# Performance work log

Measured on AMD Instinct MI355X. Metric: run time of the kernel, lower is better.

The kernel has to match this reference:

```python
import jax, jax.numpy as jnp
import numpy as np

LEAK = 0.2

def leaky(x):
    return jnp.where(x > 0, x, LEAK * x)

def relu(x):
    return jnp.maximum(x, 0)

def conv1d(x, w):
    # x [B,Cin,L], w [Cout,Cin,3], stride 1, padding 1
    return jax.lax.conv_general_dilated(x, w, (1,), [(1, 1)],
        dimension_numbers=('NCH', 'OIH', 'NCH'))

def conv2d(x, w, pad, dil=1, groups=1):
    return jax.lax.conv_general_dilated(x, w, (1, 1), [(pad, pad), (pad, pad)],
        rhs_dilation=(dil, dil), feature_group_count=groups,
        dimension_numbers=('NCHW', 'OIHW', 'NCHW'))

def bn2d(x, p, eps=1e-5):
    # p: [4,C] = gamma, beta, running_mean, running_var (eval-mode BN)
    g, b, m, v = p
    s = (1, -1, 1, 1)
    return (x - m.reshape(s)) * (g.reshape(s) / jnp.sqrt(v.reshape(s) + eps)) + b.reshape(s)

def layernorm(x, g, b, eps=1e-5):
    mu = x.mean(-1, keepdims=True)
    var = ((x - mu) ** 2).mean(-1, keepdims=True)
    return (x - mu) / jnp.sqrt(var + eps) * g + b

def l2n(x, axis, eps):
    n = jnp.sqrt((x * x).sum(axis, keepdims=True))
    return x / jnp.maximum(n, eps)


def setup_inputs() -> dict:
    key = jax.random.key(0)
    B, C, H, W = 4, 64, 48, 48
    D, Fn, T, V = 256, 8, 4, 16
    E = 16  # orthogonal prototype embed dim
    ks = iter(jax.random.split(key, 64))
    def rn(shape, s=0.05):
        return jax.random.normal(next(ks), shape, jnp.float32) * s
    def bnp(c):
        return jnp.stack([1.0 + rn((c,), 0.1), rn((c,), 0.1), rn((c,), 0.1), 1.0 + jnp.abs(rn((c,), 0.1))])
    return dict(
        basis_vector_bank=jax.random.normal(next(ks), (T, V, D), jnp.float32),
        task_f=jax.random.normal(next(ks), (B, C, 16, 16), jnp.float32),
        img_f=jax.random.normal(next(ks), (B, C, H, W), jnp.float32),
        protos=jax.random.normal(next(ks), (T, E), jnp.float32),
        tA_w1=rn((E // 4, 1, 3)), tA_w2=rn((E // 2, E // 4, 3)),
        iA_w=rn((E // 2, C, 3, 3)), iA_bn=bnp(E // 2),
        at_w1=rn((E, Fn // 2 * E)), at_b1=rn((Fn // 2 * E,)),
        at_ln_g=jnp.ones((Fn // 2 * E,)), at_ln_b=jnp.zeros((Fn // 2 * E,)),
        at_w2=rn((Fn // 2 * E, Fn * E)), at_b2=rn((Fn * E,)),
        bv_t1=rn((D // 4, 1, 3)), bv_t2=rn((D // 2, D // 4, 3)),
        bv_ic1=rn((D // 4, C, 3, 3)), bv_bn1=bnp(D // 4),
        bv_ic2=rn((D // 2, D // 4, 3, 3)), bv_bn2=bnp(D // 2),
        bv_w1=rn((D, D // 4)), bv_b1=rn((D // 4,)),
        bv_ln_g=jnp.ones((D // 4,)), bv_ln_b=jnp.zeros((D // 4,)),
        bv_w2=rn((D // 4, D)), bv_b2=rn((D,)),
        m1_w1=rn((D, D // 4)), m1_b1=rn((D // 4,)),
        m1_ln_g=jnp.ones((D // 4,)), m1_ln_b=jnp.zeros((D // 4,)),
        m1_w2=rn((D // 4, C * C)), m1_b2=rn((C * C,)),
        m3_w1=rn((D, D // 4)), m3_b1=rn((D // 4,)),
        m3_ln_g=jnp.ones((D // 4,)), m3_ln_b=jnp.zeros((D // 4,)),
        m3_w2=rn((D // 4, 9 * C * C)), m3_b2=rn((9 * C * C,)),
        blr_bn=bnp(C),
        zc_w=rn((C, C, 1, 1), 0.01), zc_b=rn((C,), 0.01),
    )


def _forward(basis_vector_bank, task_f, img_f, protos, tA_w1, tA_w2, iA_w, iA_bn,
             at_w1, at_b1, at_ln_g, at_ln_b, at_w2, at_b2,
             bv_t1, bv_t2, bv_ic1, bv_bn1, bv_ic2, bv_bn2,
             bv_w1, bv_b1, bv_ln_g, bv_ln_b, bv_w2, bv_b2,
             m1_w1, m1_b1, m1_ln_g, m1_ln_b, m1_w2, m1_b2,
             m3_w1, m3_b1, m3_ln_g, m3_ln_b, m3_w2, m3_b2,
             blr_bn, zc_w, zc_b):
    T, V, D = basis_vector_bank.shape
    B, C, H, W = img_f.shape
    E = protos.shape[1]
    Fn = at_w2.shape[1] // E
    tau = 0.5

    # --- A2SI routing features ---
    xt = task_f.reshape(B, 1, -1)
    t1 = conv1d(leaky(conv1d(xt, tA_w1)), tA_w2).mean(-1)          # [B,E/2]
    i1 = leaky(bn2d(conv2d(img_f, iA_w, 1), iA_bn)).mean((2, 3))   # [B,E/2]
    f1 = jnp.concatenate([t1, i1], axis=1)                         # [B,E]
    h = relu(layernorm(f1 @ at_w1 + at_b1, at_ln_g, at_ln_b))
    tif = (h @ at_w2 + at_b2).reshape(B, E, Fn)                    # [B,E,F]
    logits = jnp.einsum('te,bef->bft', l2n(protos, -1, 1e-8), l2n(tif, 1, 1e-8))  # [B,F,T]

    # hard gumbel-softmax (straight-through), fixed noise key for determinism
    u = jax.random.uniform(jax.random.key(42), logits.shape, jnp.float32, 1e-10, 1.0)
    g = -jnp.log(-jnp.log(u))
    y = jax.nn.softmax((logits + g) / tau, axis=-1)
    idx = jnp.argmax(y, axis=-1)                                   # [B,F]
    y_hard = jax.nn.one_hot(idx, T, dtype=y.dtype)
    set_type = y_hard + y - jax.lax.stop_gradient(y)

    bank_flat = basis_vector_bank.reshape(T, V * D)
    sbvb = jnp.einsum('bft,tk->bfk', set_type, bank_flat).reshape(B, Fn, V, D)

    # --- BasisV_filter: filter feature ---
    xt2 = task_f.reshape(B, C, -1)
    rms = jnp.sqrt((xt2 ** 2).mean((1, 2), keepdims=True))
    xt2 = (xt2 / (rms + 1e-8)).reshape(B, 1, -1)
    te = conv1d(leaky(conv1d(xt2, bv_t1)), bv_t2).mean(-1)         # [B,D/2]
    ie = leaky(bn2d(conv2d(img_f, bv_ic1, 1), bv_bn1))
    ie = leaky(bn2d(conv2d(ie, bv_ic2, 1), bv_bn2)).mean((2, 3))   # [B,D/2]
    ff = jnp.concatenate([te, ie], axis=1)                         # [B,D]
    ff = relu(layernorm(ff @ bv_w1 + bv_b1, bv_ln_g, bv_ln_b)) @ bv_w2 + bv_b2

    # --- per-(batch,type) group gather/top-k/scatter, vectorized ---
    # group bank = bank of first filter with that type (hard one-hot -> type's bank)
    occ = idx[:, None, :] == jnp.arange(T)[None, :, None]          # [B,T,F]
    first = jnp.argmax(occ, axis=-1)                               # [B,T]
    Bg = jnp.take_along_axis(sbvb, first[:, :, None, None], axis=1)  # [B,T,V,D]
    # all rows of Q within a group are identical (filter_f expanded over F),
    # so S.max(0) == cosine(ff[b], Bg[b,t])
    scores = jnp.einsum('bd,btvd->btv', l2n(ff, -1, 1e-12), l2n(Bg, -1, 1e-12))
    order = jnp.argsort(-scores, axis=-1)                          # [B,T,V] topk order
    lt = jnp.tril(jnp.ones((Fn, Fn), bool), -1)                    # j < i
    rank = ((idx[:, :, None] == idx[:, None, :]) & lt).sum(-1)     # position in group
    bidx = jnp.arange(B)[:, None]
    sel = order[bidx, idx, rank]                                   # [B,F]
    bvf = Bg[bidx, idx, sel]                                       # [B,F,D]

    # --- per-filter dynamic convolutions ---
    w1 = relu(layernorm(bvf @ m1_w1 + m1_b1, m1_ln_g, m1_ln_b)) @ m1_w2 + m1_b2
    w1 = w1.reshape(B, Fn, C, C)                                   # [B,F,out,in]
    w3 = relu(layernorm(bvf @ m3_w1 + m3_b1, m3_ln_g, m3_ln_b)) @ m3_w2 + m3_b2
    w3 = w3.reshape(B * Fn, C, C, 3, 3)

    dp0 = jnp.einsum('bfoc,bchw->bfohw', w1, img_f)                # 1x1 branch
    xin = jnp.broadcast_to(img_f[:, None], (B, Fn, C, H, W)).reshape(1, B * Fn * C, H, W)
    ker = w3.reshape(B * Fn * C, C, 3, 3)
    dpd = [conv2d(xin, ker, d, dil=d, groups=B * Fn).reshape(B, Fn, C, H, W)
           for d in (1, 2, 3)]                                     # same-padded dilated 3x3
    t_ = idx[:, :, None, None, None]
    dp = jnp.where(t_ == 0, dp0, jnp.where(t_ == 1, dpd[0],
         jnp.where(t_ == 2, dpd[1], dpd[2])))                      # [B,F,C,H,W]

    x = leaky(bn2d(dp.reshape(B * Fn, C, H, W), blr_bn)).reshape(B, Fn, C, H, W).mean(1)
    a = conv2d(x, zc_w, 0) + zc_b.reshape(1, -1, 1, 1)
    return a + img_f


@jax.jit
def reference(basis_vector_bank, task_f, img_f, protos, tA_w1, tA_w2, iA_w, iA_bn,
              at_w1, at_b1, at_ln_g, at_ln_b, at_w2, at_b2,
              bv_t1, bv_t2, bv_ic1, bv_bn1, bv_ic2, bv_bn2,
              bv_w1, bv_b1, bv_ln_g, bv_ln_b, bv_w2, bv_b2,
              m1_w1, m1_b1, m1_ln_g, m1_ln_b, m1_w2, m1_b2,
              m3_w1, m3_b1, m3_ln_g, m3_ln_b, m3_w2, m3_b2,
              blr_bn, zc_w, zc_b):
    return _forward(basis_vector_bank, task_f, img_f, protos, tA_w1, tA_w2, iA_w, iA_bn,
                    at_w1, at_b1, at_ln_g, at_ln_b, at_w2, at_b2,
                    bv_t1, bv_t2, bv_ic1, bv_bn1, bv_ic2, bv_bn2,
                    bv_w1, bv_b1, bv_ln_g, bv_ln_b, bv_w2, bv_b2,
                    m1_w1, m1_b1, m1_ln_g, m1_ln_b, m1_w2, m1_b2,
                    m3_w1, m3_b1, m3_ln_g, m3_ln_b, m3_w2, m3_b2,
                    blr_bn, zc_w, zc_b)
```

## Files before the change

kernel.cpp:

```cpp
#include <hip/hip_runtime.h>
#include <math.h>

#define LEAKC 0.2f

#define NB 4
#define NC 64
#define LLEN 16384
#define HW 2304
#define PP 54
#define PHW 2916
#define SLABP 72
#define CP 72
#define IE1C 50

typedef __attribute__((ext_vector_type(8))) short short8;
typedef __attribute__((ext_vector_type(4))) float floatx4;

__device__ __forceinline__ float leaky(float x){ return x > 0.f ? x : LEAKC*x; }

__device__ __forceinline__ float wave_sum64(float v){
  for(int off=32;off;off>>=1) v += __shfl_xor(v,off);
  return v;
}

__device__ __forceinline__ unsigned short f2bf(float x){
  unsigned u=__float_as_uint(x);
  unsigned r=u+0x7FFFu+((u>>16)&1u);
  return (unsigned short)(r>>16);
}

__device__ __forceinline__ void threefry2x32(unsigned k0, unsigned k1, unsigned& x0, unsigned& x1){
  unsigned ks0=k0, ks1=k1, ks2=k0^k1^0x1BD11BDAu;
  x0+=ks0; x1+=ks1;
  const int rot0[4]={13,15,26,6};
  const int rot1[4]={17,29,16,24};
#define TF_APPLY(rr) {for(int r=0;r<4;r++){x0+=x1; x1=(x1<<rr[r])|(x1>>(32-rr[r])); x1^=x0;}}
  TF_APPLY(rot0); x0+=ks1; x1+=ks2+1u;
  TF_APPLY(rot1); x0+=ks2; x1+=ks0+2u;
  TF_APPLY(rot0); x0+=ks0; x1+=ks1+3u;
  TF_APPLY(rot1); x0+=ks1; x1+=ks2+4u;
  TF_APPLY(rot0); x0+=ks2; x1+=ks0+5u;
#undef TF_APPLY
}

__device__ __forceinline__ float jax_uniform128(int i){
  unsigned x0=0u, x1=(unsigned)i;
  threefry2x32(0u,42u,x0,x1);
  unsigned bits = x0 ^ x1;
  unsigned fb=(bits>>9)|0x3f800000u;
  float f=__uint_as_float(fb)-1.0f;
  float u=f*(1.0f-1e-10f)+1e-10f;
  return fmaxf(1e-10f,u);
}

__global__ __launch_bounds__(256) void k_pre(const float* __restrict__ task_f,
                      const float* __restrict__ w1A, const float* __restrict__ w1B,
                      float* __restrict__ totApart, float* __restrict__ a0A, float* __restrict__ aLA,
                      float* __restrict__ totBpart, float* __restrict__ a0B, float* __restrict__ aLB,
                      float* __restrict__ rmspart,
                      const float* __restrict__ img,
                      const float* __restrict__ w1, const float* __restrict__ w2,
                      const float* __restrict__ wa,
                      unsigned short* __restrict__ imgTP,
                      unsigned short* __restrict__ W1T, unsigned short* __restrict__ W2T,
                      unsigned short* __restrict__ WAT,
                      const float* __restrict__ mw1, const float* __restrict__ mw3,
                      const float* __restrict__ bvw1p, const float* __restrict__ bvw2p,
                      const float* __restrict__ bvt2p, const float* __restrict__ atw2p,
                      const float* __restrict__ bankp,
                      const float* __restrict__ m1w2p, const float* __restrict__ m3w2p,
                      const float* __restrict__ zcwp,
                      float* __restrict__ warm){
  if(blockIdx.x<256){
    int b=blockIdx.x>>6, seg=blockIdx.x&63;
    const float* x=task_f+b*LLEN;
    float tA[4]={0,0,0,0};
    float tB[64];
#pragma unroll
    for(int c=0;c<64;c++) tB[c]=0.f;
    float sq=0.f;
    int l=seg*256+threadIdx.x;
    {
      float xm=(l>0)?x[l-1]:0.f;
      float xc=x[l];
      float xp=(l<LLEN-1)?x[l+1]:0.f;
      sq=xc*xc;
#pragma unroll
      for(int c=0;c<4;c++){
        float a=leaky(w1A[c*3+0]*xm + w1A[c*3+1]*xc + w1A[c*3+2]*xp);
        tA[c]=a;
        if(l==0) a0A[b*4+c]=a;
        if(l==LLEN-1) aLA[b*4+c]=a;
      }
#pragma unroll
      for(int c=0;c<64;c++){
        float a=leaky(w1B[c*3+0]*xm + w1B[c*3+1]*xc + w1B[c*3+2]*xp);
        tB[c]=a;
        if(l==0) a0B[b*64+c]=a;
        if(l==LLEN-1) aLB[b*64+c]=a;
      }
    }
    sq=wave_sum64(sq);
#pragma unroll
    for(int c=0;c<4;c++) tA[c]=wave_sum64(tA[c]);
#pragma unroll
    for(int c=0;c<64;c++){
      float v=tB[c];
      for(int off=32;off;off>>=1) v+=__shfl_down(v,off);
      tB[c]=v;
    }
    __shared__ float redB[4][64];
    __shared__ float redA[4][4];
    __shared__ float redQ[4];
    int wave=threadIdx.x>>6, lane=threadIdx.x&63;
    if(lane==0){
#pragma unroll
      for(int c=0;c<64;c++) redB[wave][c]=tB[c];
#pragma unroll
      for(int c=0;c<4;c++) redA[wave][c]=tA[c];
      redQ[wave]=sq;
    }
    __syncthreads();
    if(threadIdx.x<64){
      float s=redB[0][threadIdx.x]+redB[1][threadIdx.x]+redB[2][threadIdx.x]+redB[3][threadIdx.x];
      totBpart[(size_t)(b*64+seg)*64+threadIdx.x]=s;
    } else if(threadIdx.x<68){
      int c=threadIdx.x-64;
      totApart[(b*64+seg)*4+c]=redA[0][c]+redA[1][c]+redA[2][c]+redA[3][c];
    } else if(threadIdx.x==68){
      rmspart[b*64+seg]=redQ[0]+redQ[1]+redQ[2]+redQ[3];
    }
  } else if(blockIdx.x<400){
    int blk=blockIdx.x-256;
    int b=blk/36, t=blk%36;
    int p0=t*64;
    __shared__ float tile[64][65];
    int pp=threadIdx.x&63, c4=threadIdx.x>>6;
    for(int r=0;r<16;r++){
      int c=c4*16+r;
      tile[c][pp]=img[(b*64+c)*HW + p0+pp];
    }
    __syncthreads();
    int pxl=threadIdx.x>>2, cg=(threadIdx.x&3)*16;
    unsigned out[8];
#pragma unroll
    for(int q=0;q<8;q++){
      unsigned lo=f2bf(tile[cg+2*q][pxl]);
      unsigned hi=f2bf(tile[cg+2*q+1][pxl]);
      out[q]=lo|(hi<<16);
    }
    int px=p0+pxl;
    int h=px/48, w=px-h*48;
    int poff=(h+3)*PP+(w+3);
    unsigned* dst=(unsigned*)(imgTP + ((size_t)(b*PHW+poff))*64 + cg);
#pragma unroll
    for(int q=0;q<8;q++) dst[q]=out[q];
  } else if(blockIdx.x<868){
    int n=(blockIdx.x-400)*256+threadIdx.x;
    if(n<9*64*64){
      int tap=n>>12, oc=(n>>6)&63, c=n&63;
      W1T[n]=f2bf(w1[oc*576+c*9+tap]);
    } else if(n<9*64*64+9*128*64){
      int m=n-9*64*64;
      int tap=m/8192, r=m-tap*8192, oc=r>>6, c=r&63;
      W2T[m]=f2bf(w2[oc*576+c*9+tap]);
    } else {
      int q=n-9*64*64-9*128*64;
      if(q<9*16*64){
        int tap=q>>10, r=q&1023, o=r>>6, c=r&63;
        WAT[q]=(o<8)?f2bf(wa[o*576+c*9+tap]):(unsigned short)0;
      }
    }
  } else if(blockIdx.x<932){
    int t=(blockIdx.x-868)*256+threadIdx.x;
    float a=0.f;
    for(int i=t;i*16<16384;i+=16384) a+=mw1[i*16];
    for(int i=t;i*16<16384;i+=16384) a+=mw3[i*16];
    for(int i=t;i*16<16384;i+=16384) a+=bvw1p[i*16];
    for(int i=t;i*16<16384;i+=16384) a+=bvw2p[i*16];
    for(int i=t;i*16<24576;i+=16384) a+=bvt2p[i*16];
    for(int i=t;i*16<8192;i+=16384) a+=atw2p[i*16];
    for(int i=t;i*16<16384;i+=16384) a+=bankp[i*16];
    for(int i=t;i*16<262144;i+=16384) a+=m1w2p[i*16];
    for(int i=t;i*16<2359296;i+=16384) a+=m3w2p[i*16];
    for(int i=t;i*16<4096;i+=16384) a+=zcwp[i*16];
    warm[t&1023]=a;
  } else {
    int id=(blockIdx.x-932)*256+threadIdx.x;
    uint4 z=make_uint4(0,0,0,0);
    for(int cch=id;cch<19584;cch+=4096){
      int ck=cch&7, pxid=cch>>3;
      int b=pxid/612, p=pxid-b*612;
      int h,w;
      if(p<324){ int r=p/54; w=p-r*54; h=(r<3)?r:(r+48); }
      else { int q=p-324; int r2=q/6; int cc=q-r2*6; h=3+r2; w=(cc<3)?cc:(cc+48); }
      *(uint4*)(imgTP + ((size_t)(b*PHW + h*PP + w))*64 + ck*8)=z;
    }
  }
}

__global__ __launch_bounds__(512) void k_conv12(const unsigned short* __restrict__ imgTP,
                        const unsigned short* __restrict__ W1T,
                        const unsigned short* __restrict__ W2T,
                        const unsigned short* __restrict__ WAT,
                        const float* __restrict__ bn1, const float* __restrict__ bn2,
                        const float* __restrict__ bnA,
                        float* __restrict__ iepart, float* __restrict__ i1part){
  int tid=threadIdx.x;
  int lane=tid&63, wv=tid>>6;
  int n0=lane&15, kg=lane>>4;
  if(blockIdx.x<96){
    int blk=blockIdx.x;
    int b=blk/24, hp=blk-b*24;
    int h0=hp*2;
    __shared__ unsigned short slab[6*54*SLABP];
    __shared__ unsigned short ie1[4*IE1C*CP];
    {
      const unsigned short* ibase=imgTP+((size_t)b*PHW+(size_t)(h0+1)*PP)*64;
      for(int e=tid;e<6*54*8;e+=512){
        int rr=e/(54*8), rem=e-rr*54*8, w=rem>>3, ck=rem&7;
        uint4 v=*(const uint4*)(ibase+((size_t)(rr*PP+w))*64+ck*8);
        *(uint4*)(slab+(rr*54+w)*SLABP+ck*8)=v;
      }
      if(tid<64){
        int br=tid>>4, cq=(tid>>3)&1, ck=tid&7;
        *(uint4*)(ie1+((size_t)(br*IE1C+(cq?49:0)))*CP+ck*8)=make_uint4(0,0,0,0);
      }
    }
    __syncthreads();
    {
      int mt=wv&3, rh=wv>>2;
      floatx4 acc[2][3];
#pragma unroll
      for(int rr=0;rr<2;rr++)
#pragma unroll
        for(int nt=0;nt<3;nt++) acc[rr][nt]=(floatx4){0.f,0.f,0.f,0.f};
#pragma unroll
      for(int ti=0;ti<3;ti++){
#pragma unroll
        for(int tj=0;tj<3;tj++){
          int tap=ti*3+tj;
          const unsigned short* Ab=W1T+(size_t)tap*4096;
#pragma unroll
          for(int c0=0;c0<64;c0+=32){
            short8 a=*(const short8*)(Ab+((mt*16+n0)*64+c0+kg*8));
#pragma unroll
            for(int rr=0;rr<2;rr++){
              int sr=rh*2+rr+ti;
#pragma unroll
              for(int nt=0;nt<3;nt++){
                int sc=nt*16+n0+tj+2;
                short8 bv=*(const short8*)(slab+(sr*54+sc)*SLABP+c0+kg*8);
                acc[rr][nt]=__builtin_amdgcn_mfma_f32_16x16x32_bf16(a,bv,acc[rr][nt],0,0,0);
              }
            }
          }
        }
      }
      int obase=mt*16+kg*4;
      float scale[4],m_[4],be_[4];
#pragma unroll
      for(int reg=0;reg<4;reg++){
        int o=obase+reg;
        scale[reg]=bn1[o]/sqrtf(bn1[192+o]+1e-5f);
        m_[reg]=bn1[128+o]; be_[reg]=bn1[64+o];
      }
#pragma unroll
      for(int rr=0;rr<2;rr++){
        int br=rh*2+rr;
        bool rv=((unsigned)(h0-1+br))<48u;
#pragma unroll
        for(int nt=0;nt<3;nt++){
          float v0=rv?leaky((acc[rr][nt][0]-m_[0])*scale[0]+be_[0]):0.f;
          float v1=rv?leaky((acc[rr][nt][1]-m_[1])*scale[1]+be_[1]):0.f;
          float v2=rv?leaky((acc[rr][nt][2]-m_[2])*scale[2]+be_[2]):0.f;
          float v3=rv?leaky((acc[rr][nt][3]-m_[3])*scale[3]+be_[3]):0.f;
          unsigned w0=f2bf(v0)|((unsigned)f2bf(v1)<<16);
          unsigned w1=f2bf(v2)|((unsigned)f2bf(v3)<<16);
          uint2 pk={w0,w1};
          *(uint2*)(ie1+((size_t)(br*IE1C+(nt*16+1+n0)))*CP+obase)=pk;
        }
      }
    }
    __syncthreads();
    {
      int mt2=wv;
      floatx4 acc[6];
#pragma unroll
      for(int i=0;i<6;i++) acc[i]=(floatx4){0.f,0.f,0.f,0.f};
#pragma unroll
      for(int ti=0;ti<3;ti++){
#pragma unroll
        for(int tj=0;tj<3;tj++){
          int tap=ti*3+tj;
          const unsigned short* Ab=W2T+(size_t)tap*8192;
#pragma unroll
          for(int c0=0;c0<64;c0+=32){
            short8 a=*(const short8*)(Ab+((mt2*16+n0)*64+c0+kg*8));
#pragma unroll
            for(int rr=0;rr<2;rr++){
              int sr=rr+ti;
#pragma unroll
              for(int wc=0;wc<3;wc++){
                int q=wc*16+n0+tj;
                short8 bv=*(const short8*)(ie1+((size_t)(sr*IE1C+q))*CP+c0+kg*8);
                acc[rr*3+wc]=__builtin_amdgcn_mfma_f32_16x16x32_bf16(a,bv,acc[rr*3+wc],0,0,0);
              }
            }
          }
        }
      }
      int obase=mt2*16+kg*4;
#pragma unroll
      for(int reg=0;reg<4;reg++){
        int o=obase+reg;
        float scale=bn2[o]/sqrtf(bn2[384+o]+1e-5f);
        float m_=bn2[256+o], be_=bn2[128+o];
        float part=0;
#pragma unroll
        for(int i=0;i<6;i++) part+=leaky((acc[i][reg]-m_)*scale+be_);
        for(int off=1;off<16;off<<=1) part+=__shfl_xor(part,off);
        if(n0==0) iepart[(b*24+hp)*128+o]=part*(1.f/2304.f);
      }
    }
  } else {
    int blk2=blockIdx.x-96;
    int b=blk2/3, hg=blk2-b*3;
    int hp=hg*8+wv;
    int h0=hp*2;
    const unsigned short* ib=imgTP+(size_t)b*PHW*64;
    floatx4 acc[6];
#pragma unroll
    for(int i=0;i<6;i++) acc[i]=(floatx4){0.f,0.f,0.f,0.f};
#pragma unroll
    for(int ti=0;ti<3;ti++){
#pragma unroll
      for(int tj=0;tj<3;tj++){
        int tap=ti*3+tj;
        const unsigned short* Ab=WAT+(size_t)tap*1024;
#pragma unroll
        for(int c0=0;c0<64;c0+=32){
          short8 a=*(const short8*)(Ab+(n0*64+c0+kg*8));
#pragma unroll
          for(int rr=0;rr<2;rr++){
            int r=h0+rr+ti-1+3;
#pragma unroll
            for(int wc=0;wc<3;wc++){
              int w=wc*16+n0+tj-1+3;
              short8 bv=*(const short8*)(ib+((size_t)(r*PP+w)*64+c0+kg*8));
              acc[rr*3+wc]=__builtin_amdgcn_mfma_f32_16x16x32_bf16(a,bv,acc[rr*3+wc],0,0,0);
            }
          }
        }
      }
    }
    int obase=kg*4;
#pragma unroll
    for(int reg=0;reg<4;reg++){
      int o=obase+reg;
      float part=0;
      if(o<8){
        float scale=bnA[o]/sqrtf(bnA[24+o]+1e-5f);
        float m_=bnA[16+o], be_=bnA[8+o];
#pragma unroll
        for(int i=0;i<6;i++) part+=leaky((acc[i][reg]-m_)*scale+be_);
      }
      for(int off=1;off<16;off<<=1) part+=__shfl_xor(part,off);
      if(n0==0 && o<8) i1part[(b*24+hp)*8+o]=part*(1.f/2304.f);
    }
  }
}

__global__ __launch_bounds__(512,1) void k_mid(
    const float* __restrict__ totApart, const float* __restrict__ a0A, const float* __restrict__ aLA,
    const float* __restrict__ totBpart, const float* __restrict__ a0B, const float* __restrict__ aLB,
    const float* __restrict__ rmspart,
    const float* __restrict__ tA_w2, const float* __restrict__ bv_t2,
    const float* __restrict__ i1part, const float* __restrict__ iepart,
    const float* __restrict__ at_w1, const float* __restrict__ at_b1,
    const float* __restrict__ at_ln_g, const float* __restrict__ at_ln_b,
    const float* __restrict__ at_w2, const float* __restrict__ at_b2,
    const float* __restrict__ protos,
    const float* __restrict__ bv_w1, const float* __restrict__ bv_b1,
    const float* __restrict__ bv_ln_g, const float* __restrict__ bv_ln_b,
    const float* __restrict__ bv_w2, const float* __restrict__ bv_b2,
    const float* __restrict__ bank,
    const float* __restrict__ m1_w1, const float* __restrict__ m1_b1,
    const float* __restrict__ m1_g,  const float* __restrict__ m1_bb,
    const float* __restrict__ m3_w1, const float* __restrict__ m3_b1,
    const float* __restrict__ m3_g,  const float* __restrict__ m3_bb,
    int* __restrict__ idxo, float* __restrict__ hid1, float* __restrict__ hid3){
  int b=blockIdx.x;
  int tid=threadIdx.x;
  int lane=tid&63, wv=tid>>6;
  const float invL=1.0f/16384.0f;
  __shared__ float sT[64], s0[64], sL[64];
  __shared__ float red8[64][9];
  __shared__ float iered[128], i1red[8];
  __shared__ float totA_s[4];
  __shared__ float rms_s;
  __shared__ float part[512];
  __shared__ float te_s[128], t1_s[8];
  __shared__ float f1[16], h[64], tif[128], tifn[128], tden[8], pden[4], pn[64], z[32];
  __shared__ int sidx[8], sfirst[4], srank[8], rows[8];
  __shared__ float fbuf[256], hh[64], ffn_s[256], finv_s;
  __shared__ float scores[64];
  __shared__ int order[64];
  __shared__ float bvf[2048];

  {
    int c8=tid>>3, g8=tid&7;
    float s8=0;
#pragma unroll
    for(int seg=g8*8;seg<g8*8+8;seg++) s8+=totBpart[(size_t)(b*64+seg)*64+c8];
    red8[c8][g8]=s8;
  }
  if(tid>=64 && tid<128){
    int t=tid-64;
    s0[t]=a0B[b*64+t]; sL[t]=aLB[b*64+t];
  } else if(tid>=128 && tid<192){
    float v=rmspart[b*64+(tid-128)];
    v=wave_sum64(v);
    if(tid==128) rms_s=v;
  } else if(tid>=192 && tid<196){
    int c=tid-192;
    float s=0;
#pragma unroll 8
    for(int seg=0;seg<64;seg++) s+=totApart[(b*64+seg)*4+c];
    totA_s[c]=s;
  } else if(tid>=256 && tid<384){
    int c=tid-256;
    float s=0;
#pragma unroll 8
    for(int g=0;g<24;g++) s+=iepart[(b*24+g)*128+c];
    iered[c]=s;
  } else if(tid>=384 && tid<392){
    int f=tid-384;
    float s=0;
#pragma unroll
    for(int g=0;g<24;g++) s+=i1part[(b*24+g)*8+f];
    i1red[f]=s;
  }
  __syncthreads();
  if(tid<64){
    float s=0;
#pragma unroll
    for(int g=0;g<8;g++) s+=red8[tid][g];
    sT[tid]=s;
  }
  __syncthreads();
  float scB=1.0f/(sqrtf(rms_s*invL)+1e-8f);
  if(tid<256){
    int c2=tid&127, h2=tid>>7;
    const float* wr=bv_t2+c2*192;
    float s=0;
    for(int c1=h2*32;c1<h2*32+32;c1+=8){
      float4 q[6];
      const float4* r4=(const float4*)(wr+c1*3);
#pragma unroll
      for(int u=0;u<6;u++) q[u]=r4[u];
      const float* qq=(const float*)q;
#pragma unroll
      for(int u=0;u<8;u++){
        int c=c1+u;
        float T=sT[c], A0=s0[c], AL=sL[c];
        s += qq[u*3+0]*(T-AL) + qq[u*3+1]*T + qq[u*3+2]*(T-A0);
      }
    }
    part[tid]=s;
  } else if(tid>=384 && tid<392){
    int c2=tid-384;
    float s=0;
    for(int c1=0;c1<4;c1++){
      float T=totA_s[c1], A0=a0A[b*4+c1], AL=aLA[b*4+c1];
      const float* w=&tA_w2[(c2*4+c1)*3];
      s += w[0]*(T-AL) + w[1]*T + w[2]*(T-A0);
    }
    t1_s[c2]=s*invL;
  }
  __syncthreads();
  if(tid<128) te_s[tid]=(part[tid]+part[tid+128])*invL*scB;
  __syncthreads();

  if(tid<8) f1[tid]=t1_s[tid];
  else if(tid<16) f1[tid]=i1red[tid-8];
  __syncthreads();
  if(tid<64){
    float s=at_b1[lane];
#pragma unroll
    for(int i=0;i<16;i++) s+=f1[i]*at_w1[i*64+lane];
    float mu=wave_sum64(s)*(1.f/64.f);
    float d=s-mu;
    float var=wave_sum64(d*d)*(1.f/64.f);
    h[lane]=fmaxf(d*(1.0f/sqrtf(var+1e-5f))*at_ln_g[lane]+at_ln_b[lane],0.f);
  }
  __syncthreads();
  if(tid<256){
    int n=tid&127, h2=tid>>7;
    float a0=0,a1=0;
    for(int k=h2*32;k<h2*32+32;k+=2){
      a0+=h[k]*at_w2[k*128+n];
      a1+=h[k+1]*at_w2[(k+1)*128+n];
    }
    part[tid]=a0+a1;
  }
  __syncthreads();
  if(tid<128) tif[tid]=at_b2[tid]+part[tid]+part[tid+128];
  __syncthreads();
  if(tid<8){
    int f=tid;
    float ss=0; for(int e=0;e<16;e++){float v=tif[e*8+f]; ss+=v*v;}
    tden[f]=fmaxf(sqrtf(ss),1e-8f);
  } else if(tid<12){
    int t=tid-8;
    float ss=0; for(int e=0;e<16;e++){float v=protos[t*16+e]; ss+=v*v;}
    pden[t]=fmaxf(sqrtf(ss),1e-8f);
  }
  __syncthreads();
  if(tid<128) tifn[tid]=tif[tid]/tden[tid&7];
  if(tid<64) pn[tid]=protos[tid]/pden[tid>>4];
  __syncthreads();
  if(tid<32){
    int f=tid>>2, t=tid&3;
    float ss=0;
#pragma unroll
    for(int e=0;e<16;e++) ss+=pn[t*16+e]*tifn[e*8+f];
    float u=jax_uniform128(b*32+f*4+t);
    float g=-logf(-logf(u));
    z[tid]=ss+g;
  }
  __syncthreads();
  if(tid<8){
    float best=z[tid*4]; int bi=0;
    for(int t=1;t<4;t++){ float v=z[tid*4+t]; if(v>best){best=v;bi=t;} }
    sidx[tid]=bi;
  }
  __syncthreads();
  if(tid<4){
    int t=tid;
    int fi=0;
    for(int f=7;f>=0;f--) if(sidx[f]==t) fi=f;
    sfirst[t]=fi;
  } else if(tid<12){
    int f=tid-4;
    int c=0; for(int f2=0;f2<f;f2++) if(sidx[f2]==sidx[f]) c++;
    srank[f]=c;
  }
  __syncthreads();

  if(tid<128) fbuf[tid]=te_s[tid];
  else if(tid<256) fbuf[tid]=iered[tid-128];
  __syncthreads();
  if(tid<256){
    int l64=tid&63, q=tid>>6;
    float a0=0,a1=0,a2=0,a3=0;
    for(int k=q*64;k<q*64+64;k+=4){
      a0+=fbuf[k]  *bv_w1[k*64+l64];
      a1+=fbuf[k+1]*bv_w1[(k+1)*64+l64];
      a2+=fbuf[k+2]*bv_w1[(k+2)*64+l64];
      a3+=fbuf[k+3]*bv_w1[(k+3)*64+l64];
    }
    part[tid]=((a0+a1)+(a2+a3));
  }
  __syncthreads();
  if(tid<64){
    float s=bv_b1[lane]+part[lane]+part[64+lane]+part[128+lane]+part[192+lane];
    float mu=wave_sum64(s)*(1.f/64.f);
    float d=s-mu;
    float var=wave_sum64(d*d)*(1.f/64.f);
    hh[lane]=fmaxf(d*(1.0f/sqrtf(var+1e-5f))*bv_ln_g[lane]+bv_ln_b[lane],0.f);
  }
  __syncthreads();
  {
    int n=tid&255, h2=tid>>8;
    float a0=0,a1=0;
    for(int k=h2*32;k<h2*32+32;k+=2){
      a0+=hh[k]*bv_w2[k*256+n];
      a1+=hh[k+1]*bv_w2[(k+1)*256+n];
    }
    part[tid]=a0+a1;
  }
  __syncthreads();
  if(tid<256) ffn_s[tid]=bv_b2[tid]+part[tid]+part[tid+256];
  __syncthreads();
  if(tid<64){
    float sq=0;
#pragma unroll
    for(int u=0;u<4;u++){ float v=ffn_s[u*64+lane]; sq+=v*v; }
    sq=wave_sum64(sq);
    if(lane==0) finv_s=1.0f/fmaxf(sqrtf(sq),1e-12f);
  }
  __syncthreads();
  if(tid<256) ffn_s[tid]*=finv_s;
  __syncthreads();

  if(tid<128){
    int it=tid&63, h2=tid>>6;
    int t=it>>4, v=it&15;
    int tt=sidx[sfirst[t]];
    const float4* row=(const float4*)(bank+(tt*16+v)*256);
    float sa=0,na=0;
    for(int d4=h2*32;d4<h2*32+32;d4++){
      float4 r=row[d4];
      const float* fp=&ffn_s[d4*4];
      sa+=fp[0]*r.x+fp[1]*r.y+fp[2]*r.z+fp[3]*r.w;
      na+=r.x*r.x+r.y*r.y+r.z*r.z+r.w*r.w;
    }
    part[tid]=sa;
    part[256+tid]=na;
  }
  __syncthreads();
  if(tid<64) scores[tid]=(part[tid]+part[tid+64])/fmaxf(sqrtf(part[256+tid]+part[320+tid]),1e-12f);
  __syncthreads();
  if(tid<4){
    const float* sc=&scores[tid*16];
    unsigned used=0;
    for(int pk=0;pk<16;pk++){
      int best=-1; float bv=-1e30f;
      for(int v2=0;v2<16;v2++){
        if(used&(1u<<v2)) continue;
        float vv=sc[v2];
        if(best<0||vv>bv){bv=vv;best=v2;}
      }
      used|=1u<<best;
      order[tid*16+pk]=best;
    }
  }
  __syncthreads();
  if(tid<8){
    int t=sidx[tid];
    int v=order[t*16+srank[tid]];
    rows[tid]=t*16+v;
    idxo[b*8+tid]=t;
  }
  __syncthreads();

  for(int ii=tid;ii<2048;ii+=512){
    int r=ii>>8, d=ii&255;
    bvf[ii]=bank[rows[r]*256+d];
  }
  __syncthreads();
  {
    int r=wv;
    const float* bp=&bvf[r*256];
    float a0=0,a1=0,a2=0,a3=0;
    float c0=0,c1=0,c2=0,c3=0;
    for(int d=0;d<256;d+=4){
      float b0=bp[d],b1=bp[d+1],b2=bp[d+2],b3=bp[d+3];
      a0+=b0*m1_w1[d*64+lane];
      a1+=b1*m1_w1[(d+1)*64+lane];
      a2+=b2*m1_w1[(d+2)*64+lane];
      a3+=b3*m1_w1[(d+3)*64+lane];
      c0+=b0*m3_w1[d*64+lane];
      c1+=b1*m3_w1[(d+1)*64+lane];
      c2+=b2*m3_w1[(d+2)*64+lane];
      c3+=b3*m3_w1[(d+3)*64+lane];
    }
    float s1=m1_b1[lane]+((a0+a1)+(a2+a3));
    float s3=m3_b1[lane]+((c0+c1)+(c2+c3));
    float mu=wave_sum64(s1)*(1.f/64.f);
    float dd=s1-mu;
    float var=wave_sum64(dd*dd)*(1.f/64.f);
    hid1[(b*8+r)*64+lane]=fmaxf(dd*(1.0f/sqrtf(var+1e-5f))*m1_g[lane]+m1_bb[lane],0.f);
    mu=wave_sum64(s3)*(1.f/64.f);
    dd=s3-mu;
    var=wave_sum64(dd*dd)*(1.f/64.f);
    hid3[(b*8+r)*64+lane]=fmaxf(dd*(1.0f/sqrtf(var+1e-5f))*m3_g[lane]+m3_bb[lane],0.f);
  }
}

__global__ __launch_bounds__(256) void k_heads(const float* __restrict__ hid1, const float* __restrict__ hid3,
                        const float* __restrict__ w2a, const float* __restrict__ b2a,
                        const float* __restrict__ w2b, const float* __restrict__ b2b,
                        unsigned short* __restrict__ A1, unsigned short* __restrict__ A3){
  __shared__ float hl[2048];
  if(blockIdx.x<16){
    int n=blockIdx.x*256+threadIdx.x;
    float wcol[64];
#pragma unroll
    for(int k=0;k<64;k++) wcol[k]=w2a[k*4096+n];
    float bb=b2a[n];
    for(int i=threadIdx.x;i<2048;i+=256) hl[i]=hid1[i];
    __syncthreads();
    for(int bf=0;bf<32;bf++){
      float s=bb;
#pragma unroll
      for(int k=0;k<64;k++) s+=hl[bf*64+k]*wcol[k];
      A1[bf*4096+n]=f2bf(s);
    }
  } else {
    int n=(blockIdx.x-16)*256+threadIdx.x;
    float wcol[64];
#pragma unroll
    for(int k=0;k<64;k++) wcol[k]=w2b[(size_t)k*36864+n];
    float bb=b2b[n];
    for(int i=threadIdx.x;i<2048;i+=256) hl[i]=hid3[i];
    __syncthreads();
    int o=n/576, rem=n-o*576;
    int c=rem/9, tap=rem-c*9;
    size_t base=((size_t)tap*64+o)*64+c;
    for(int bf=0;bf<32;bf++){
      float s=bb;
#pragma unroll
      for(int k=0;k<64;k++) s+=hl[bf*64+k]*wcol[k];
      A3[(size_t)bf*9*4096+base]=f2bf(s);
    }
  }
}

__global__ __launch_bounds__(512) void k_dynF(const unsigned short* __restrict__ imgTP,
                       const unsigned short* __restrict__ A1, const unsigned short* __restrict__ A3,
                       const int* __restrict__ idx, const float* __restrict__ bn,
                       const float* __restrict__ zc_w, const float* __restrict__ zc_b,
                       const float* __restrict__ img, float* __restrict__ out){
  int blk=blockIdx.x;
  int b=blk/48, r0=blk-b*48;
  int tid=threadIdx.x;
  int lane=tid&63, w8=tid>>6;
  int mt=w8&3, fh=w8>>2;
  int n0=lane&15, kg=lane>>4;
  __shared__ unsigned short slab[7*54*SLABP];
  __shared__ float xl[64*50];
  __shared__ float zl[4096];
  int tts[4];
#pragma unroll
  for(int i=0;i<4;i++) tts[i]=idx[b*8+fh*4+i];
  int obase=mt*16+kg*4;
  float scale[4],m_[4],be_[4];
#pragma unroll
  for(int reg=0;reg<4;reg++){
    int o=obase+reg;
    scale[reg]=bn[o]/sqrtf(bn[192+o]+1e-5f);
    m_[reg]=bn[128+o]; be_[reg]=bn[64+o];
  }
  for(int i=tid;i<4096;i+=512) zl[i]=zc_w[i];
  for(int i=tid;i<3200;i+=512) xl[i]=0.f;
  {
    const unsigned short* ibase=imgTP+((size_t)b*PHW+(size_t)r0*PP)*64;
    for(int e=tid;e<7*54*8;e+=512){
      int rr=e/(54*8), rem=e-rr*54*8, w=rem>>3, ck=rem&7;
      uint4 v=*(const uint4*)(ibase + ((size_t)(rr*PP+w))*64 + ck*8);
      *(uint4*)(slab + (rr*54+w)*SLABP + ck*8)=v;
    }
  }
  __syncthreads();
  float xsum[3][4];
#pragma unroll
  for(int wc=0;wc<3;wc++)
#pragma unroll
    for(int reg=0;reg<4;reg++) xsum[wc][reg]=0.f;
#pragma unroll
  for(int fi=0;fi<4;fi++){
    int f=fh*4+fi;
    int bf=b*8+f;
    int tt=tts[fi];
    floatx4 acc[3];
#pragma unroll
    for(int i=0;i<3;i++) acc[i]=(floatx4){0.f,0.f,0.f,0.f};
    if(tt==0){
      const unsigned short* Ab=A1+(size_t)bf*4096;
#pragma unroll
      for(int c0=0;c0<64;c0+=32){
        short8 a=*(const short8*)(Ab+((mt*16+n0)*64+c0+kg*8));
#pragma unroll
        for(int wc=0;wc<3;wc++){
          short8 bv=*(const short8*)(slab + (3*54 + wc*16+n0+3)*SLABP + c0+kg*8);
          acc[wc]=__builtin_amdgcn_mfma_f32_16x16x32_bf16(a,bv,acc[wc],0,0,0);
        }
      }
    } else {
      int d=tt;
      const unsigned short* A3b=A3+(size_t)bf*9*4096;
#pragma unroll
      for(int ti=0;ti<3;ti++){
        int lr=d*(ti-1)+3;
#pragma unroll
        for(int tj=0;tj<3;tj++){
          int tap=ti*3+tj;
          int dw=d*(tj-1)+3;
          const unsigned short* Ab=A3b+(size_t)tap*4096;
#pragma unroll
          for(int c0=0;c0<64;c0+=32){
            short8 a=*(const short8*)(Ab+((mt*16+n0)*64+c0+kg*8));
#pragma unroll
            for(int wc=0;wc<3;wc++){
              short8 bv=*(const short8*)(slab + (lr*54 + wc*16+n0+dw)*SLABP + c0+kg*8);
              acc[wc]=__builtin_amdgcn_mfma_f32_16x16x32_bf16(a,bv,acc[wc],0,0,0);
            }
          }
        }
      }
    }
#pragma unroll
    for(int wc=0;wc<3;wc++)
#pragma unroll
      for(int reg=0;reg<4;reg++)
        xsum[wc][reg]+=leaky((acc[wc][reg]-m_[reg])*scale[reg]+be_[reg]);
  }
#pragma unroll
  for(int wc=0;wc<3;wc++)
#pragma unroll
    for(int reg=0;reg<4;reg++)
      atomicAdd(&xl[(obase+reg)*50 + wc*16+n0], xsum[wc][reg]*0.125f);
  __syncthreads();
  size_t base=(size_t)b*64*HW + r0*48;
  for(int e=tid;e<3072;e+=512){
    int o=e/48, px=e-o*48;
    float s=zc_b[o];
#pragma unroll
    for(int c=0;c<64;c++) s+=zl[o*64+c]*xl[c*50+px];
    size_t a=base+(size_t)o*HW+px;
    out[a]=s+img[a];
  }
}

extern "C" void kernel_launch(void* const* d_in, const int* in_sizes, int n_in,
                              void* d_out, int out_size, void* d_ws, size_t ws_size,
                              hipStream_t stream){
  const float* bank   =(const float*)d_in[0];
  const float* task_f =(const float*)d_in[1];
  const float* img_f  =(const float*)d_in[2];
  const float* protos =(const float*)d_in[3];
  const float* tA_w1  =(const float*)d_in[4];
  const float* tA_w2  =(const float*)d_in[5];
  const float* iA_w   =(const float*)d_in[6];
  const float* iA_bn  =(const float*)d_in[7];
  const float* at_w1  =(const float*)d_in[8];
  const float* at_b1  =(const float*)d_in[9];
  const float* at_ln_g=(const float*)d_in[10];
  const float* at_ln_b=(const float*)d_in[11];
  const float* at_w2  =(const float*)d_in[12];
  const float* at_b2  =(const float*)d_in[13];
  const float* bv_t1  =(const float*)d_in[14];
  const float* bv_t2  =(const float*)d_in[15];
  const float* bv_ic1 =(const float*)d_in[16];
  const float* bv_bn1 =(const float*)d_in[17];
  const float* bv_ic2 =(const float*)d_in[18];
  const float* bv_bn2 =(const float*)d_in[19];
  const float* bv_w1  =(const float*)d_in[20];
  const float* bv_b1  =(const float*)d_in[21];
  const float* bv_ln_g=(const float*)d_in[22];
  const float* bv_ln_b=(const float*)d_in[23];
  const float* bv_w2  =(const float*)d_in[24];
  const float* bv_b2  =(const float*)d_in[25];
  const float* m1_w1  =(const float*)d_in[26];
  const float* m1_b1  =(const float*)d_in[27];
  const float* m1_ln_g=(const float*)d_in[28];
  const float* m1_ln_b=(const float*)d_in[29];
  const float* m1_w2  =(const float*)d_in[30];
  const float* m1_b2  =(const float*)d_in[31];
  const float* m3_w1  =(const float*)d_in[32];
  const float* m3_b1  =(const float*)d_in[33];
  const float* m3_ln_g=(const float*)d_in[34];
  const float* m3_ln_b=(const float*)d_in[35];
  const float* m3_w2  =(const float*)d_in[36];
  const float* m3_b2  =(const float*)d_in[37];
  const float* blr_bn =(const float*)d_in[38];
  const float* zc_w   =(const float*)d_in[39];
  const float* zc_b   =(const float*)d_in[40];

  float* ws=(float*)d_ws;
  float* totApart=ws+0;
  float* a0A  =ws+1024;
  float* aLA  =ws+1040;
  float* totBpart=ws+1056;
  float* a0B  =ws+17440;
  float* aLB  =ws+17696;
  float* rmspart=ws+17952;
  float* i1part =ws+18208;
  float* iepart =ws+18976;
  int*   idxp   =(int*)(ws+31264);
  float* hid1=ws+31296;
  float* hid3=ws+33344;
  unsigned short* A1p  =(unsigned short*)(ws+35392);
  unsigned short* A3p  =(unsigned short*)(ws+100928);
  unsigned short* imgTP=(unsigned short*)(ws+690752);
  unsigned short* W1Tp =(unsigned short*)(ws+1064000);
  unsigned short* W2Tp =(unsigned short*)(ws+1082432);
  unsigned short* WATp =(unsigned short*)(ws+1119296);
  float* warm =ws+1123904;

  k_pre<<<948,256,0,stream>>>(task_f, tA_w1, bv_t1,
                              totApart, a0A, aLA, totBpart, a0B, aLB, rmspart,
                              img_f, bv_ic1, bv_ic2, iA_w, imgTP, W1Tp, W2Tp, WATp,
                              m1_w1, m3_w1, bv_w1, bv_w2, bv_t2, at_w2, bank,
                              m1_w2, m3_w2, zc_w, warm);
  k_conv12<<<108,512,0,stream>>>(imgTP, W1Tp, W2Tp, WATp, bv_bn1, bv_bn2, iA_bn,
                                 iepart, i1part);
  k_mid<<<4,512,0,stream>>>(totApart,a0A,aLA,totBpart,a0B,aLB, rmspart, tA_w2, bv_t2,
                            i1part, iepart,
                            at_w1, at_b1, at_ln_g, at_ln_b, at_w2, at_b2, protos,
                            bv_w1, bv_b1, bv_ln_g, bv_ln_b, bv_w2, bv_b2, bank,
                            m1_w1, m1_b1, m1_ln_g, m1_ln_b,
                            m3_w1, m3_b1, m3_ln_g, m3_ln_b,
                            idxp, hid1, hid3);
  k_heads<<<160,256,0,stream>>>(hid1, hid3, m1_w2, m1_b2, m3_w2, m3_b2, A1p, A3p);
  k_dynF<<<192,512,0,stream>>>(imgTP, A1p, A3p, idxp, blr_bn, zc_w, zc_b, img_f, (float*)d_out);

  (void)in_sizes; (void)n_in; (void)out_size; (void)ws_size;
}
```

Baseline: 268.4 us.

## Fuse conv and mid kernels with atomic completion counter handoff

Merges the conv kernel and the per-batch mid kernel into one launch of 112 blocks. Conv blocks bump a device-scope counter when they finish, and the four mid blocks run the independent task-side work first, then presumably spin on the counter before reading the conv partial sums. Shared memory is unioned through one raw buffer. This removes one launch and overlaps mid-stage prologue work with the convs, at the risk of a deadlock if the mid blocks are scheduled before the conv blocks can finish, and it adds counter reset logic in the pre kernel.

New measurement: 266.1 us. About the same (-0.8%).

```diff
diff --git a/kernel.cpp b/kernel.cpp
--- a/kernel.cpp
+++ b/kernel.cpp
@@ -52,6 +52,21 @@
   float u=f*(1.0f-1e-10f)+1e-10f;
   return fmaxf(1e-10f,u);
 }
+
+struct MidSM {
+  float sT[64], s0[64], sL[64];
+  float red8[64][9];
+  float totA_s[4]; float rms_s;
+  float part[512];
+  float te_s[128], t1_s[8];
+  float f1[16], h[64], tif[128], tifn[128], tden[8], pden[4], pn[64], z[32];
+  int sidx[8], sfirst[4], srank[8], rows[8];
+  float iered[128];
+  float fbuf[256], hh[64], ffn_s[256], finv_s;
+  float scores[64];
+  int order[64];
+  float bvf[2048];
+};
 
 __global__ __launch_bounds__(256) void k_pre(const float* __restrict__ task_f,
                       const float* __restrict__ w1A, const float* __restrict__ w1B,
@@ -70,7 +85,7 @@
                       const float* __restrict__ bankp,
                       const float* __restrict__ m1w2p, const float* __restrict__ m3w2p,
                       const float* __restrict__ zcwp,
-                      float* __restrict__ warm){
+                      float* __restrict__ warm, int* __restrict__ donec){
   if(blockIdx.x<256){
     int b=blockIdx.x>>6, seg=blockIdx.x&63;
     const float* x=task_f+b*LLEN;
@@ -186,6 +201,7 @@
     for(int i=t;i*16<4096;i+=16384) a+=zcwp[i*16];
     warm[t&1023]=a;
   } else {
+    if(blockIdx.x==932 && threadIdx.x==0) *donec=0;
     int id=(blockIdx.x-932)*256+threadIdx.x;
     uint4 z=make_uint4(0,0,0,0);
     for(int cch=id;cch<19584;cch+=4096){
@@ -199,184 +215,15 @@
   }
 }
 
-__global__ __launch_bounds__(512) void k_conv12(const unsigned short* __restrict__ imgTP,
-                        const unsigned short* __restrict__ W1T,
-                        const unsigned short* __restrict__ W2T,
-                        const unsigned short* __restrict__ WAT,
-                        const float* __restrict__ bn1, const float* __restrict__ bn2,
-                        const float* __restrict__ bnA,
-                        float* __restrict__ iepart, float* __restrict__ i1part){
-  int tid=threadIdx.x;
-  int lane=tid&63, wv=tid>>6;
-  int n0=lane&15, kg=lane>>4;
-  if(blockIdx.x<96){
-    int blk=blockIdx.x;
-    int b=blk/24, hp=blk-b*24;
-    int h0=hp*2;
-    __shared__ unsigned short slab[6*54*SLABP];
-    __shared__ unsigned short ie1[4*IE1C*CP];
-    {
-      const unsigned short* ibase=imgTP+((size_t)b*PHW+(size_t)(h0+1)*PP)*64;
-      for(int e=tid;e<6*54*8;e+=512){
-        int rr=e/(54*8), rem=e-rr*54*8, w=rem>>3, ck=rem&7;
-        uint4 v=*(const uint4*)(ibase+((size_t)(rr*PP+w))*64+ck*8);
-        *(uint4*)(slab+(rr*54+w)*SLABP+ck*8)=v;
-      }
-      if(tid<64){
-        int br=tid>>4, cq=(tid>>3)&1, ck=tid&7;
-        *(uint4*)(ie1+((size_t)(br*IE1C+(cq?49:0)))*CP+ck*8)=make_uint4(0,0,0,0);
-      }
-    }
-    __syncthreads();
-    {
-      int mt=wv&3, rh=wv>>2;
-      floatx4 acc[2][3];
-#pragma unroll
-      for(int rr=0;rr<2;rr++)
-#pragma unroll
-        for(int nt=0;nt<3;nt++) acc[rr][nt]=(floatx4){0.f,0.f,0.f,0.f};
-#pragma unroll
-      for(int ti=0;ti<3;ti++){
-#pragma unroll
-        for(int tj=0;tj<3;tj++){
-          int tap=ti*3+tj;
-          const unsigned short* Ab=W1T+(size_t)tap*4096;
-#pragma unroll
-          for(int c0=0;c0<64;c0+=32){
-            short8 a=*(const short8*)(Ab+((mt*16+n0)*64+c0+kg*8));
-#pragma unroll
-            for(int rr=0;rr<2;rr++){
-              int sr=rh*2+rr+ti;
-#pragma unroll
-              for(int nt=0;nt<3;nt++){
-                int sc=nt*16+n0+tj+2;
-                short8 bv=*(const short8*)(slab+(sr*54+sc)*SLABP+c0+kg*8);
-                acc[rr][nt]=__builtin_amdgcn_mfma_f32_16x16x32_bf16(a,bv,acc[rr][nt],0,0,0);
-              }
-            }
-          }
-        }
-      }
-      int obase=mt*16+kg*4;
-      float scale[4],m_[4],be_[4];
-#pragma unroll
-      for(int reg=0;reg<4;reg++){
-        int o=obase+reg;
-        scale[reg]=bn1[o]/sqrtf(bn1[192+o]+1e-5f);
-        m_[reg]=bn1[128+o]; be_[reg]=bn1[64+o];
-      }
-#pragma unroll
-      for(int rr=0;rr<2;rr++){
-        int br=rh*2+rr;
-        bool rv=((unsigned)(h0-1+br))<48u;
-#pragma unroll
-        for(int nt=0;nt<3;nt++){
-          float v0=rv?leaky((acc[rr][nt][0]-m_[0])*scale[0]+be_[0]):0.f;
-          float v1=rv?leaky((acc[rr][nt][1]-m_[1])*scale[1]+be_[1]):0.f;
-          float v2=rv?leaky((acc[rr][nt][2]-m_[2])*scale[2]+be_[2]):0.f;
-          float v3=rv?leaky((acc[rr][nt][3]-m_[3])*scale[3]+be_[3]):0.f;
-          unsigned w0=f2bf(v0)|((unsigned)f2bf(v1)<<16);
-          unsigned w1=f2bf(v2)|((unsigned)f2bf(v3)<<16);
-          uint2 pk={w0,w1};
-          *(uint2*)(ie1+((size_t)(br*IE1C+(nt*16+1+n0)))*CP+obase)=pk;
-        }
-      }
-    }
-    __syncthreads();
-    {
-      int mt2=wv;
-      floatx4 acc[6];
-#pragma unroll
-      for(int i=0;i<6;i++) acc[i]=(floatx4){0.f,0.f,0.f,0.f};
-#pragma unroll
-      for(int ti=0;ti<3;ti++){
-#pragma unroll
-        for(int tj=0;tj<3;tj++){
-          int tap=ti*3+tj;
-          const unsigned short* Ab=W2T+(size_t)tap*8192;
-#pragma unroll
-          for(int c0=0;c0<64;c0+=32){
-            short8 a=*(const short8*)(Ab+((mt2*16+n0)*64+c0+kg*8));
-#pragma unroll
-            for(int rr=0;rr<2;rr++){
-              int sr=rr+ti;
-#pragma unroll
-              for(int wc=0;wc<3;wc++){
-                int q=wc*16+n0+tj;
-                short8 bv=*(const short8*)(ie1+((size_t)(sr*IE1C+q))*CP+c0+kg*8);
-                acc[rr*3+wc]=__builtin_amdgcn_mfma_f32_16x16x32_bf16(a,bv,acc[rr*3+wc],0,0,0);
-              }
-            }
-          }
-        }
-      }
-      int obase=mt2*16+kg*4;
-#pragma unroll
-      for(int reg=0;reg<4;reg++){
-        int o=obase+reg;
-        float scale=bn2[o]/sqrtf(bn2[384+o]+1e-5f);
-        float m_=bn2[256+o], be_=bn2[128+o];
-        float part=0;
-#pragma unroll
-        for(int i=0;i<6;i++) part+=leaky((acc[i][reg]-m_)*scale+be_);
-        for(int off=1;off<16;off<<=1) part+=__shfl_xor(part,off);
-        if(n0==0) iepart[(b*24+hp)*128+o]=part*(1.f/2304.f);
-      }
-    }
-  } else {
-    int blk2=blockIdx.x-96;
-    int b=blk2/3, hg=blk2-b*3;
-    int hp=hg*8+wv;
-    int h0=hp*2;
-    const unsigned short* ib=imgTP+(size_t)b*PHW*64;
-    floatx4 acc[6];
-#pragma unroll
-    for(int i=0;i<6;i++) acc[i]=(floatx4){0.f,0.f,0.f,0.f};
-#pragma unroll
-    for(int ti=0;ti<3;ti++){
-#pragma unroll
-      for(int tj=0;tj<3;tj++){
-        int tap=ti*3+tj;
-        const unsigned short* Ab=WAT+(size_t)tap*1024;
-#pragma unroll
-        for(int c0=0;c0<64;c0+=32){
-          short8 a=*(const short8*)(Ab+(n0*64+c0+kg*8));
-#pragma unroll
-          for(int rr=0;rr<2;rr++){
-            int r=h0+rr+ti-1+3;
-#pragma unroll
-            for(int wc=0;wc<3;wc++){
-              int w=wc*16+n0+tj-1+3;
-              short8 bv=*(const short8*)(ib+((size_t)(r*PP+w)*64+c0+kg*8));
-              acc[rr*3+wc]=__builtin_amdgcn_mfma_f32_16x16x32_bf16(a,bv,acc[rr*3+wc],0,0,0);
-            }
-          }
-        }
-      }
-    }
-    int obase=kg*4;
-#pragma unroll
-    for(int reg=0;reg<4;reg++){
-      int o=obase+reg;
-      float part=0;
-      if(o<8){
-        float scale=bnA[o]/sqrtf(bnA[24+o]+1e-5f);
-        float m_=bnA[16+o], be_=bnA[8+o];
-#pragma unroll
-        for(int i=0;i<6;i++) part+=leaky((acc[i][reg]-m_)*scale+be_);
-      }
-      for(int off=1;off<16;off<<=1) part+=__shfl_xor(part,off);
-      if(n0==0 && o<8) i1part[(b*24+hp)*8+o]=part*(1.f/2304.f);
-    }
-  }
-}
-
-__global__ __launch_bounds__(512,1) void k_mid(
+__global__ __launch_bounds__(512) void k_cm(const unsigned short* __restrict__ imgTP,
+    const unsigned short* __restrict__ W1T, const unsigned short* __restrict__ W2T,
+    const unsigned short* __restrict__ WAT,
+    const float* __restrict__ bn1, const float* __restrict__ bn2, const float* __restrict__ bnA,
+    float* __restrict__ iepart, float* __restrict__ i1part,
     const float* __restrict__ totApart, const float* __restrict__ a0A, const float* __restrict__ aLA,
     const float* __restrict__ totBpart, const float* __restrict__ a0B, const float* __restrict__ aLB,
     const float* __restrict__ rmspart,
     const float* __restrict__ tA_w2, const float* __restrict__ bv_t2,
-    const float* __restrict__ i1part, const float* __restrict__ iepart,
     const float* __restrict__ at_w1, const float* __restrict__ at_b1,
     const float* __restrict__ at_ln_g, const float* __restrict__ at_ln_b,
     const float* __restrict__ at_w2, const float* __restrict__ at_b2,
@@ -389,283 +236,442 @@
     const float* __restrict__ m1_g,  const float* __restrict__ m1_bb,
     const float* __restrict__ m3_w1, const float* __restrict__ m3_b1,
     const float* __restrict__ m3_g,  const float* __restrict__ m3_bb,
-    int* __restrict__ idxo, float* __restrict__ hid1, float* __restrict__ hid3){
-  int b=blockIdx.x;
+    int* __restrict__ idxo, float* __restrict__ hid1, float* __restrict__ hid3,
+    int* __restrict__ donec){
+  __shared__ __align__(16) char smraw[75456];
   int tid=threadIdx.x;
   int lane=tid&63, wv=tid>>6;
-  const float invL=1.0f/16384.0f;
-  __shared__ float sT[64], s0[64], sL[64];
-  __shared__ float red8[64][9];
-  __shared__ float iered[128], i1red[8];
-  __shared__ float totA_s[4];
-  __shared__ float rms_s;
-  __shared__ float part[512];
-  __shared__ float te_s[128], t1_s[8];
-  __shared__ float f1[16], h[64], tif[128], tifn[128], tden[8], pden[4], pn[64], z[32];
-  __shared__ int sidx[8], sfirst[4], srank[8], rows[8];
-  __shared__ float fbuf[256], hh[64], ffn_s[256], finv_s;
-  __shared__ float scores[64];
-  __shared__ int order[64];
-  __shared__ float bvf[2048];
-
-  {
-    int c8=tid>>3, g8=tid&7;
-    float s8=0;
-#pragma unroll
-    for(int seg=g8*8;seg<g8*8+8;seg++) s8+=totBpart[(size_t)(b*64+seg)*64+c8];
-    red8[c8][g8]=s8;
-  }
-  if(tid>=64 && tid<128){
-    int t=tid-64;
-    s0[t]=a0B[b*64+t]; sL[t]=aLB[b*64+t];
-  } else if(tid>=128 && tid<192){
-    float v=rmspart[b*64+(tid-128)];
-    v=wave_sum64(v);
-    if(tid==128) rms_s=v;
-  } else if(tid>=192 && tid<196){
-    int c=tid-192;
-    float s=0;
+  int n0=lane&15, kg=lane>>4;
+  if(blockIdx.x<96){
+    int blk=blockIdx.x;
+    int b=blk/24, hp=blk-b*24;
+    int h0=hp*2;
+    unsigned short* slab=(unsigned short*)smraw;
+    unsigned short* ie1=(unsigned short*)(smraw+46656);
+    {
+      const unsigned short* ibase=imgTP+((size_t)b*PHW+(size_t)(h0+1)*PP)*64;
+      for(int e=tid;e<6*54*8;e+=512){
+        int rr=e/(54*8), rem=e-rr*54*8, w=rem>>3, ck=rem&7;
+        uint4 v=*(const uint4*)(ibase+((size_t)(rr*PP+w))*64+ck*8);
+        *(uint4*)(slab+(rr*54+w)*SLABP+ck*8)=v;
+      }
+      if(tid<64){
+        int br=tid>>4, cq=(tid>>3)&1, ck=tid&7;
+        *(uint4*)(ie1+((size_t)(br*IE1C+(cq?49:0)))*CP+ck*8)=make_uint4(0,0,0,0);
+      }
+    }
+    __syncthreads();
+    {
+      int mt=wv&3, rh=wv>>2;
+      floatx4 acc[2][3];
+#pragma unroll
+      for(int rr=0;rr<2;rr++)
+#pragma unroll
+        for(int nt=0;nt<3;nt++) acc[rr][nt]=(floatx4){0.f,0.f,0.f,0.f};
+#pragma unroll
+      for(int ti=0;ti<3;ti++){
+#pragma unroll
+        for(int tj=0;tj<3;tj++){
+          int tap=ti*3+tj;
+          const unsigned short* Ab=W1T+(size_t)tap*4096;
+#pragma unroll
+          for(int c0=0;c0<64;c0+=32){
+            short8 a=*(const short8*)(Ab+((mt*16+n0)*64+c0+kg*8));
+#pragma unroll
+            for(int rr=0;rr<2;rr++){
+              int sr=rh*2+rr+ti;
+#pragma unroll
+              for(int nt=0;nt<3;nt++){
+                int sc=nt*16+n0+tj+2;
+                short8 bv=*(const short8*)(slab+(sr*54+sc)*SLABP+c0+kg*8);
+                acc[rr][nt]=__builtin_amdgcn_mfma_f32_16x16x32_bf16(a,bv,acc[rr][nt],0,0,0);
+              }
+            }
+          }
+        }
+      }
+      int obase=mt*16+kg*4;
+      float scale[4],m_[4],be_[4];
+#pragma unroll
+      for(int reg=0;reg<4;reg++){
+        int o=obase+reg;
+        scale[reg]=bn1[o]/sqrtf(bn1[192+o]+1e-5f);
+        m_[reg]=bn1[128+o]; be_[reg]=bn1[64+o];
+      }
+#pragma unroll
+      for(int rr=0;rr<2;rr++){
+        int br=rh*2+rr;
+        bool rv=((unsigned)(h0-1+br))<48u;
+#pragma unroll
+        for(int nt=0;nt<3;nt++){
+          float v0=rv?leaky((acc[rr][nt][0]-m_[0])*scale[0]+be_[0]):0.f;
+          float v1=rv?leaky((acc[rr][nt][1]-m_[1])*scale[1]+be_[1]):0.f;
+          float v2=rv?leaky((acc[rr][nt][2]-m_[2])*scale[2]+be_[2]):0.f;
+          float v3=rv?leaky((acc[rr][nt][3]-m_[3])*scale[3]+be_[3]):0.f;
+          unsigned w0=f2bf(v0)|((unsigned)f2bf(v1)<<16);
+          unsigned w1=f2bf(v2)|((unsigned)f2bf(v3)<<16);
+          uint2 pk={w0,w1};
+          *(uint2*)(ie1+((size_t)(br*IE1C+(nt*16+1+n0)))*CP+obase)=pk;
+        }
+      }
+    }
+    __syncthreads();
+    {
+      int mt2=wv;
+      floatx4 acc[6];
+#pragma unroll
+      for(int i=0;i<6;i++) acc[i]=(floatx4){0.f,0.f,0.f,0.f};
+#pragma unroll
+      for(int ti=0;ti<3;ti++){
+#pragma unroll
+        for(int tj=0;tj<3;tj++){
+          int tap=ti*3+tj;
+          const unsigned short* Ab=W2T+(size_t)tap*8192;
+#pragma unroll
+          for(int c0=0;c0<64;c0+=32){
+            short8 a=*(const short8*)(Ab+((mt2*16+n0)*64+c0+kg*8));
+#pragma unroll
+            for(int rr=0;rr<2;rr++){
+              int sr=rr+ti;
+#pragma unroll
+              for(int wc=0;wc<3;wc++){
+                int q=wc*16+n0+tj;
+                short8 bv=*(const short8*)(ie1+((size_t)(sr*IE1C+q))*CP+c0+kg*8);
+                acc[rr*3+wc]=__builtin_amdgcn_mfma_f32_16x16x32_bf16(a,bv,acc[rr*3+wc],0,0,0);
+              }
+            }
+          }
+        }
+      }
+      int obase=mt2*16+kg*4;
+#pragma unroll
+      for(int reg=0;reg<4;reg++){
+        int o=obase+reg;
+        float scale=bn2[o]/sqrtf(bn2[384+o]+1e-5f);
+        float m_=bn2[256+o], be_=bn2[128+o];
+        float part=0;
+#pragma unroll
+        for(int i=0;i<6;i++) part+=leaky((acc[i][reg]-m_)*scale+be_);
+        for(int off=1;off<16;off<<=1) part+=__shfl_xor(part,off);
+        if(n0==0) iepart[(b*24+hp)*128+o]=part*(1.f/2304.f);
+      }
+    }
+    __syncthreads();
+    if(tid==0) __hip_atomic_fetch_add(donec,1,__ATOMIC_RELEASE,__HIP_MEMORY_SCOPE_AGENT);
+  } else if(blockIdx.x<108){
+    int blk2=blockIdx.x-96;
+    int b=blk2/3, hg=blk2%3;
+    int hp=hg*8+wv;
+    int h0=hp*2;
+    const unsigned short* ib=imgTP+(size_t)b*PHW*64;
+    floatx4 acc[6];
+#pragma unroll
+    for(int i=0;i<6;i++) acc[i]=(floatx4){0.f,0.f,0.f,0.f};
+#pragma unroll
+    for(int ti=0;ti<3;ti++){
+#pragma unroll
+      for(int tj=0;tj<3;tj++){
+        int tap=ti*3+tj;
+        const unsigned short* Ab=WAT+(size_t)tap*1024;
+#pragma unroll
+        for(int c0=0;c0<64;c0+=32){
+          short8 a=*(const short8*)(Ab+(n0*64+c0+kg*8));
+#pragma unroll
+          for(int rr=0;rr<2;rr++){
+            int r=h0+rr+ti-1+3;
+#pragma unroll
+            for(int wc=0;wc<3;wc++){
+              int w=wc*16+n0+tj-1+3;
+              short8 bv=*(const short8*)(ib+((size_t)(r*PP+w)*64+c0+kg*8));
+              acc[rr*3+wc]=__builtin_amdgcn_mfma_f32_16x16x32_bf16(a,bv,acc[rr*3+wc],0,0,0);
+            }
+          }
+        }
+      }
+    }
+    int obase=kg*4;
+#pragma unroll
+    for(int reg=0;reg<4;reg++){
+      int o=obase+reg;
+      float part=0;
+      if(o<8){
+        float scale=bnA[o]/sqrtf(bnA[24+o]+1e-5f);
+        float m_=bnA[16+o], be_=bnA[8+o];
+#pragma unroll
+        for(int i=0;i<6;i++) part+=leaky((acc[i][reg]-m_)*scale+be_);
+      }
+      for(int off=1;off<16;off<<=1) part+=__shfl_xor(part,off);
+      if(n0==0 && o<8) i1part[(b*24+hp)*8+o]=part*(1.f/2304.f);
+    }
+    __syncthreads();
+    if(tid==0) __hip_atomic_fetch_add(donec,1,__ATOMIC_RELEASE,__HIP_MEMORY_SCOPE_AGENT);
+  } else {
+    MidSM* S=(MidSM*)smraw;
+    int b=blockIdx.x-108;
+    const float invL=1.0f/16384.0f;
+    {
+      int c8=tid>>3, g8=tid&7;
+      float s8=0;
+#pragma unroll
+      for(int seg=g8*8;seg<g8*8+8;seg++) s8+=totBpart[(size_t)(b*64+seg)*64+c8];
+      S->red8[c8][g8]=s8;
+    }
+    if(tid>=64 && tid<128){
+      int t=tid-64;
+      S->s0[t]=a0B[b*64+t]; S->sL[t]=aLB[b*64+t];
+    } else if(tid>=128 && tid<192){
+      float v=rmspart[b*64+(tid-128)];
+      v=wave_sum64(v);
+      if(tid==128) S->rms_s=v;
+    } else if(tid>=192 && tid<196){
+      int c=tid-192;
+      float s=0;
 #pragma unroll 8
-    for(int seg=0;seg<64;seg++) s+=totApart[(b*64+seg)*4+c];
-    totA_s[c]=s;
-  } else if(tid>=256 && tid<384){
-    int c=tid-256;
-    float s=0;
+      for(int seg=0;seg<64;seg++) s+=totApart[(b*64+seg)*4+c];
+      S->totA_s[c]=s;
+    }
+    __syncthreads();
+    if(tid<64){
+      float s=0;
+#pragma unroll
+      for(int g=0;g<8;g++) s+=S->red8[tid][g];
+      S->sT[tid]=s;
+    }
+    __syncthreads();
+    float scB=1.0f/(sqrtf(S->rms_s*invL)+1e-8f);
+    if(tid<256){
+      int c2=tid&127, h2=tid>>7;
+      const float* wr=bv_t2+c2*192;
+      float s=0;
+      for(int c1=h2*32;c1<h2*32+32;c1+=8){
+        float4 q[6];
+        const float4* r4=(const float4*)(wr+c1*3);
+#pragma unroll
+        for(int u=0;u<6;u++) q[u]=r4[u];
+        const float* qq=(const float*)q;
+#pragma unroll
+        for(int u=0;u<8;u++){
+          int c=c1+u;
+          float T=S->sT[c], A0=S->s0[c], AL=S->sL[c];
+          s += qq[u*3+0]*(T-AL) + qq[u*3+1]*T + qq[u*3+2]*(T-A0);
+        }
+      }
+      S->part[tid]=s;
+    } else if(tid>=384 && tid<392){
+      int c2=tid-384;
+      float s=0;
+      for(int c1=0;c1<4;c1++){
+        float T=S->totA_s[c1], A0=a0A[b*4+c1], AL=aLA[b*4+c1];
+        const float* w=&tA_w2[(c2*4+c1)*3];
+        s += w[0]*(T-AL) + w[1]*T + w[2]*(T-A0);
+      }
+      S->t1_s[c2]=s*invL;
+    }
+    __syncthreads();
+    if(tid<128) S->te_s[tid]=(S->part[tid]+S->part[tid+128])*invL*scB;
+    __syncthreads();
+    if(tid==0){
+      while(__hip_atomic_load(donec,__ATOMIC_ACQUIRE,__HIP_MEMORY_SCOPE_AGENT)<108)
+        __builtin_amdgcn_s_sleep(8);
+    }
+    __syncthreads();
+    if(tid<8) S->f1[tid]=S->t1_s[tid];
+    else if(tid<16){
+      int f=tid-8;
+      float s=0;
+#pragma unroll
+      for(int g=0;g<24;g++) s+=i1part[(b*24+g)*8+f];
+      S->f1[tid]=s;
+    } else if(tid>=256 && tid<384){
+      int c=tid-256;
+      float s=0;
 #pragma unroll 8
-    for(int g=0;g<24;g++) s+=iepart[(b*24+g)*128+c];
-    iered[c]=s;
-  } else if(tid>=384 && tid<392){
-    int f=tid-384;
-    float s=0;
-#pragma unroll
-    for(int g=0;g<24;g++) s+=i1part[(b*24+g)*8+f];
-    i1red[f]=s;
-  }
-  __syncthreads();
-  if(tid<64){
-    float s=0;
-#pragma unroll
-    for(int g=0;g<8;g++) s+=red8[tid][g];
-    sT[tid]=s;
-  }
-  __syncthreads();
-  float scB=1.0f/(sqrtf(rms_s*invL)+1e-8f);
-  if(tid<256){
-    int c2=tid&127, h2=tid>>7;
-    const float* wr=bv_t2+c2*192;
-    float s=0;
-    for(int c1=h2*32;c1<h2*32+32;c1+=8){
-      float4 q[6];
-      const float4* r4=(const float4*)(wr+c1*3);
-#pragma unroll
-      for(int u=0;u<6;u++) q[u]=r4[u];
-      const float* qq=(const float*)q;
-#pragma unroll
-      for(int u=0;u<8;u++){
-        int c=c1+u;
-        float T=sT[c], A0=s0[c], AL=sL[c];
-        s += qq[u*3+0]*(T-AL) + qq[u*3+1]*T + qq[u*3+2]*(T-A0);
-      }
-    }
-    part[tid]=s;
-  } else if(tid>=384 && tid<392){
-    int c2=tid-384;
-    float s=0;
-    for(int c1=0;c1<4;c1++){
-      float T=totA_s[c1], A0=a0A[b*4+c1], AL=aLA[b*4+c1];
-      const float* w=&tA_w2[(c2*4+c1)*3];
-      s += w[0]*(T-AL) + w[1]*T + w[2]*(T-A0);
-    }
-    t1_s[c2]=s*invL;
-  }
-  __syncthreads();
-  if(tid<128) te_s[tid]=(part[tid]+part[tid+128])*invL*scB;
-  __syncthreads();
-
-  if(tid<8) f1[tid]=t1_s[tid];
-  else if(tid<16) f1[tid]=i1red[tid-8];
-  __syncthreads();
-  if(tid<64){
-    float s=at_b1[lane];
-#pragma unroll
-    for(int i=0;i<16;i++) s+=f1[i]*at_w1[i*64+lane];
-    float mu=wave_sum64(s)*(1.f/64.f);
-    float d=s-mu;
-    float var=wave_sum64(d*d)*(1.f/64.f);
-    h[lane]=fmaxf(d*(1.0f/sqrtf(var+1e-5f))*at_ln_g[lane]+at_ln_b[lane],0.f);
-  }
-  __syncthreads();
-  if(tid<256){
-    int n=tid&127, h2=tid>>7;
-    float a0=0,a1=0;
-    for(int k=h2*32;k<h2*32+32;k+=2){
-      a0+=h[k]*at_w2[k*128+n];
-      a1+=h[k+1]*at_w2[(k+1)*128+n];
-    }
-    part[tid]=a0+a1;
-  }
-  __syncthreads();
-  if(tid<128) tif[tid]=at_b2[tid]+part[tid]+part[tid+128];
-  __syncthreads();
-  if(tid<8){
-    int f=tid;
-    float ss=0; for(int e=0;e<16;e++){float v=tif[e*8+f]; ss+=v*v;}
-    tden[f]=fmaxf(sqrtf(ss),1e-8f);
-  } else if(tid<12){
-    int t=tid-8;
-    float ss=0; for(int e=0;e<16;e++){float v=protos[t*16+e]; ss+=v*v;}
-    pden[t]=fmaxf(sqrtf(ss),1e-8f);
-  }
-  __syncthreads();
-  if(tid<128) tifn[tid]=tif[tid]/tden[tid&7];
-  if(tid<64) pn[tid]=protos[tid]/pden[tid>>4];
-  __syncthreads();
-  if(tid<32){
-    int f=tid>>2, t=tid&3;
-    float ss=0;
-#pragma unroll
-    for(int e=0;e<16;e++) ss+=pn[t*16+e]*tifn[e*8+f];
-    float u=jax_uniform128(b*32+f*4+t);
-    float g=-logf(-logf(u));
-    z[tid]=ss+g;
-  }
-  __syncthreads();
-  if(tid<8){
-    float best=z[tid*4]; int bi=0;
-    for(int t=1;t<4;t++){ float v=z[tid*4+t]; if(v>best){best=v;bi=t;} }
-    sidx[tid]=bi;
-  }
-  __syncthreads();
-  if(tid<4){
-    int t=tid;
-    int fi=0;
-    for(int f=7;f>=0;f--) if(sidx[f]==t) fi=f;
-    sfirst[t]=fi;
-  } else if(tid<12){
-    int f=tid-4;
-    int c=0; for(int f2=0;f2<f;f2++) if(sidx[f2]==sidx[f]) c++;
-    srank[f]=c;
-  }
-  __syncthreads();
-
-  if(tid<128) fbuf[tid]=te_s[tid];
-  else if(tid<256) fbuf[tid]=iered[tid-128];
-  __syncthreads();
-  if(tid<256){
-    int l64=tid&63, q=tid>>6;
-    float a0=0,a1=0,a2=0,a3=0;
-    for(int k=q*64;k<q*64+64;k+=4){
-      a0+=fbuf[k]  *bv_w1[k*64+l64];
-      a1+=fbuf[k+1]*bv_w1[(k+1)*64+l64];
-      a2+=fbuf[k+2]*bv_w1[(k+2)*64+l64];
-      a3+=fbuf[k+3]*bv_w1[(k+3)*64+l64];
-    }
-    part[tid]=((a0+a1)+(a2+a3));
-  }
-  __syncthreads();
-  if(tid<64){
-    float s=bv_b1[lane]+part[lane]+part[64+lane]+part[128+lane]+part[192+lane];
-    float mu=wave_sum64(s)*(1.f/64.f);
-    float d=s-mu;
-    float var=wave_sum64(d*d)*(1.f/64.f);
-    hh[lane]=fmaxf(d*(1.0f/sqrtf(var+1e-5f))*bv_ln_g[lane]+bv_ln_b[lane],0.f);
-  }
-  __syncthreads();
-  {
-    int n=tid&255, h2=tid>>8;
-    float a0=0,a1=0;
-    for(int k=h2*32;k<h2*32+32;k+=2){
-      a0+=hh[k]*bv_w2[k*256+n];
-      a1+=hh[k+1]*bv_w2[(k+1)*256+n];
-    }
-    part[tid]=a0+a1;
-  }
-  __syncthreads();
-  if(tid<256) ffn_s[tid]=bv_b2[tid]+part[tid]+part[tid+256];
-  __syncthreads();
-  if(tid<64){
-    float sq=0;
-#pragma unroll
-    for(int u=0;u<4;u++){ float v=ffn_s[u*64+lane]; sq+=v*v; }
-    sq=wave_sum64(sq);
-    if(lane==0) finv_s=1.0f/fmaxf(sqrtf(sq),1e-12f);
-  }
-  __syncthreads();
-  if(tid<256) ffn_s[tid]*=finv_s;
-  __syncthreads();
-
-  if(tid<128){
-    int it=tid&63, h2=tid>>6;
-    int t=it>>4, v=it&15;
-    int tt=sidx[sfirst[t]];
-    const float4* row=(const float4*)(bank+(tt*16+v)*256);
-    float sa=0,na=0;
-    for(int d4=h2*32;d4<h2*32+32;d4++){
-      float4 r=row[d4];
-      const float* fp=&ffn_s[d4*4];
-      sa+=fp[0]*r.x+fp[1]*r.y+fp[2]*r.z+fp[3]*r.w;
-      na+=r.x*r.x+r.y*r.y+r.z*r.z+r.w*r.w;
-    }
-    part[tid]=sa;
-    part[256+tid]=na;
-  }
-  __syncthreads();
-  if(tid<64) scores[tid]=(part[tid]+part[tid+64])/fmaxf(sqrtf(part[256+tid]+part[320+tid]),1e-12f);
-  __syncthreads();
-  if(tid<4){
-    const float* sc=&scores[tid*16];
-    unsigned used=0;
-    for(int pk=0;pk<16;pk++){
-      int best=-1; float bv=-1e30f;
-      for(int v2=0;v2<16;v2++){
-        if(used&(1u<<v2)) continue;
-        float vv=sc[v2];
-        if(best<0||vv>bv){bv=vv;best=v2;}
-      }
-      used|=1u<<best;
-      order[tid*16+pk]=best;
-    }
-  }
-  __syncthreads();
-  if(tid<8){
-    int t=sidx[tid];
-    int v=order[t*16+srank[tid]];
-    rows[tid]=t*16+v;
-    idxo[b*8+tid]=t;
-  }
-  __syncthreads();
-
-  for(int ii=tid;ii<2048;ii+=512){
-    int r=ii>>8, d=ii&255;
-    bvf[ii]=bank[rows[r]*256+d];
-  }
-  __syncthreads();
-  {
-    int r=wv;
-    const float* bp=&bvf[r*256];
-    float a0=0,a1=0,a2=0,a3=0;
-    float c0=0,c1=0,c2=0,c3=0;
-    for(int d=0;d<256;d+=4){
-      float b0=bp[d],b1=bp[d+1],b2=bp[d+2],b3=bp[d+3];
-      a0+=b0*m1_w1[d*64+lane];
-      a1+=b1*m1_w1[(d+1)*64+lane];
-      a2+=b2*m1_w1[(d+2)*64+lane];
-      a3+=b3*m1_w1[(d+3)*64+lane];
-      c0+=b0*m3_w1[d*64+lane];
-      c1+=b1*m3_w1[(d+1)*64+lane];
-      c2+=b2*m3_w1[(d+2)*64+lane];
-      c3+=b3*m3_w1[(d+3)*64+lane];
-    }
-    float s1=m1_b1[lane]+((a0+a1)+(a2+a3));
-    float s3=m3_b1[lane]+((c0+c1)+(c2+c3));
-    float mu=wave_sum64(s1)*(1.f/64.f);
-    float dd=s1-mu;
-    float var=wave_sum64(dd*dd)*(1.f/64.f);
-    hid1[(b*8+r)*64+lane]=fmaxf(dd*(1.0f/sqrtf(var+1e-5f))*m1_g[lane]+m1_bb[lane],0.f);
-    mu=wave_sum64(s3)*(1.f/64.f);
-    dd=s3-mu;
-    var=wave_sum64(dd*dd)*(1.f/64.f);
-    hid3[(b*8+r)*64+lane]=fmaxf(dd*(1.0f/sqrtf(var+1e-5f))*m3_g[lane]+m3_bb[lane],0.f);
+      for(int g=0;g<24;g++) s+=iepart[(b*24+g)*128+c];
+      S->iered[c]=s;
+    }
+    __syncthreads();
+    if(tid<64){
+      float s=at_b1[lane];
+#pragma unroll
+      for(int i=0;i<16;i++) s+=S->f1[i]*at_w1[i*64+lane];
+      float mu=wave_sum64(s)*(1.f/64.f);
+      float d=s-mu;
+      float var=wave_sum64(d*d)*(1.f/64.f);
+      S->h[lane]=fmaxf(d*(1.0f/sqrtf(var+1e-5f))*at_ln_g[lane]+at_ln_b[lane],0.f);
+    }
+    __syncthreads();
+    if(tid<256){
+      int n=tid&127, h2=tid>>7;
+      float a0=0,a1=0;
+      for(int k=h2*32;k<h2*32+32;k+=2){
+        a0+=S->h[k]*at_w2[k*128+n];
+        a1+=S->h[k+1]*at_w2[(k+1)*128+n];
+      }
+      S->part[tid]=a0+a1;
+    }
+    __syncthreads();
+    if(tid<128) S->tif[tid]=at_b2[tid]+S->part[tid]+S->part[tid+128];
+    __syncthreads();
+    if(tid<8){
+      int f=tid;
+      float ss=0; for(int e=0;e<16;e++){float v=S->tif[e*8+f]; ss+=v*v;}
+      S->tden[f]=fmaxf(sqrtf(ss),1e-8f);
+    } else if(tid<12){
+      int t=tid-8;
+      float ss=0; for(int e=0;e<16;e++){float v=protos[t*16+e]; ss+=v*v;}
+      S->pden[t]=fmaxf(sqrtf(ss),1e-8f);
+    }
+    __syncthreads();
+    if(tid<128) S->tifn[tid]=S->tif[tid]/S->tden[tid&7];
+    if(tid<64) S->pn[tid]=protos[tid]/S->pden[tid>>4];
+    __syncthreads();
+    if(tid<32){
+      int f=tid>>2, t=tid&3;
+      float ss=0;
+#pragma unroll
+      for(int e=0;e<16;e++) ss+=S->pn[t*16+e]*S->tifn[e*8+f];
+      float u=jax_uniform128(b*32+f*4+t);
+      float g=-logf(-logf(u));
+      S->z[tid]=ss+g;
+    }
+    __syncthreads();
+    if(tid<8){
+      float best=S->z[tid*4]; int bi=0;
+      for(int t=1;t<4;t++){ float v=S->z[tid*4+t]; if(v>best){best=v;bi=t;} }
+      S->sidx[tid]=bi;
+    }
+    __syncthreads();
+    if(tid<4){
+      int t=tid;
+      int fi=0;
+      for(int f=7;f>=0;f--) if(S->sidx[f]==t) fi=f;
+      S->sfirst[t]=fi;
+    } else if(tid<12){
+      int f=tid-4;
+      int c=0; for(int f2=0;f2<f;f2++) if(S->sidx[f2]==S->sidx[f]) c++;
+      S->srank[f]=c;
+    }
+    __syncthreads();
+
+    if(tid<128) S->fbuf[tid]=S->te_s[tid];
+    else if(tid<256) S->fbuf[tid]=S->iered[tid-128];
+    __syncthreads();
+    if(tid<256){
+      int l64=tid&63, q=tid>>6;
+      float a0=0,a1=0,a2=0,a3=0;
+      for(int k=q*64;k<q*64+64;k+=4){
+        a0+=S->fbuf[k]  *bv_w1[k*64+l64];
+        a1+=S->fbuf[k+1]*bv_w1[(k+1)*64+l64];
+        a2+=S->fbuf[k+2]*bv_w1[(k+2)*64+l64];
+        a3+=S->fbuf[k+3]*bv_w1[(k+3)*64+l64];
+      }
+      S->part[tid]=((a0+a1)+(a2+a3));
+    }
+    __syncthreads();
+    if(tid<64){
+      float s=bv_b1[lane]+S->part[lane]+S->part[64+lane]+S->part[128+lane]+S->part[192+lane];
+      float mu=wave_sum64(s)*(1.f/64.f);
+      float d=s-mu;
+      float var=wave_sum64(d*d)*(1.f/64.f);
+      S->hh[lane]=fmaxf(d*(1.0f/sqrtf(var+1e-5f))*bv_ln_g[lane]+bv_ln_b[lane],0.f);
+    }
+    __syncthreads();
+    {
+      int n=tid&255, h2=tid>>8;
+      float a0=0,a1=0;
+      for(int k=h2*32;k<h2*32+32;k+=2){
+        a0+=S->hh[k]*bv_w2[k*256+n];
+        a1+=S->hh[k+1]*bv_w2[(k+1)*256+n];
+      }
+      S->part[tid]=a0+a1;
+    }
+    __syncthreads();
+    if(tid<256) S->ffn_s[tid]=bv_b2[tid]+S->part[tid]+S->part[tid+256];
+    __syncthreads();
+    if(tid<64){
+      float sq=0;
+#pragma unroll
+      for(int u=0;u<4;u++){ float v=S->ffn_s[u*64+lane]; sq+=v*v; }
+      sq=wave_sum64(sq);
+      if(lane==0) S->finv_s=1.0f/fmaxf(sqrtf(sq),1e-12f);
+    }
+    __syncthreads();
+    if(tid<256) S->ffn_s[tid]*=S->finv_s;
+    __syncthreads();
+
+    if(tid<128){
+      int it=tid&63, h2=tid>>6;
+      int t=it>>4, v=it&15;
+      int tt=S->sidx[S->sfirst[t]];
+      const float4* row=(const float4*)(bank+(tt*16+v)*256);
+      float sa=0,na=0;
+      for(int d4=h2*32;d4<h2*32+32;d4++){
+        float4 r=row[d4];
+        const float* fp=&S->ffn_s[d4*4];
+        sa+=fp[0]*r.x+fp[1]*r.y+fp[2]*r.z+fp[3]*r.w;
+        na+=r.x*r.x+r.y*r.y+r.z*r.z+r.w*r.w;
+      }
+      S->part[tid]=sa;
+      S->part[256+tid]=na;
+    }
+    __syncthreads();
+    if(tid<64) S->scores[tid]=(S->part[tid]+S->part[tid+64])/fmaxf(sqrtf(S->part[256+tid]+S->part[320+tid]),1e-12f);
+    __syncthreads();
+    if(tid<4){
+      const float* sc=&S->scores[tid*16];
+      unsigned used=0;
+      for(int pk=0;pk<16;pk++){
+        int best=-1; float bv=-1e30f;
+        for(int v2=0;v2<16;v2++){
+          if(used&(1u<<v2)) continue;
+          float vv=sc[v2];
+          if(best<0||vv>bv){bv=vv;best=v2;}
+        }
+        used|=1u<<best;
+        S->order[tid*16+pk]=best;
+      }
+    }
+    __syncthreads();
+    if(tid<8){
+      int t=S->sidx[tid];
+      int v=S->order[t*16+S->srank[tid]];
+      S->rows[tid]=t*16+v;
+      idxo[b*8+tid]=t;
+    }
+    __syncthreads();
+
+    for(int ii=tid;ii<2048;ii+=512){
+      int r=ii>>8, d=ii&255;
+      S->bvf[ii]=bank[S->rows[r]*256+d];
+    }
+    __syncthreads();
+    {
+      int r=wv;
+      const float* bp=&S->bvf[r*256];
+      float a0=0,a1=0,a2=0,a3=0;
+      float c0=0,c1=0,c2=0,c3=0;
+      for(int d=0;d<256;d+=4){
+        float b0=bp[d],b1=bp[d+1],b2=bp[d+2],b3=bp[d+3];
+        a0+=b0*m1_w1[d*64+lane];
+        a1+=b1*m1_w1[(d+1)*64+lane];
+        a2+=b2*m1_w1[(d+2)*64+lane];
+        a3+=b3*m1_w1[(d+3)*64+lane];
+        c0+=b0*m3_w1[d*64+lane];
+        c1+=b1*m3_w1[(d+1)*64+lane];
+        c2+=b2*m3_w1[(d+2)*64+lane];
+        c3+=b3*m3_w1[(d+3)*64+lane];
+      }
+      float s1=m1_b1[lane]+((a0+a1)+(a2+a3));
+      float s3=m3_b1[lane]+((c0+c1)+(c2+c3));
+      float mu=wave_sum64(s1)*(1.f/64.f);
+      float dd=s1-mu;
+      float var=wave_sum64(dd*dd)*(1.f/64.f);
+      hid1[(b*8+r)*64+lane]=fmaxf(dd*(1.0f/sqrtf(var+1e-5f))*m1_g[lane]+m1_bb[lane],0.f);
+      mu=wave_sum64(s3)*(1.f/64.f);
+      dd=s3-mu;
+      var=wave_sum64(dd*dd)*(1.f/64.f);
+      hid3[(b*8+r)*64+lane]=fmaxf(dd*(1.0f/sqrtf(var+1e-5f))*m3_g[lane]+m3_bb[lane],0.f);
+    }
   }
 }
 
@@ -879,21 +885,22 @@
   unsigned short* W2Tp =(unsigned short*)(ws+1082432);
   unsigned short* WATp =(unsigned short*)(ws+1119296);
   float* warm =ws+1123904;
+  int*   donec=(int*)(ws+1124928);
 
   k_pre<<<948,256,0,stream>>>(task_f, tA_w1, bv_t1,
                               totApart, a0A, aLA, totBpart, a0B, aLB, rmspart,
                               img_f, bv_ic1, bv_ic2, iA_w, imgTP, W1Tp, W2Tp, WATp,
                               m1_w1, m3_w1, bv_w1, bv_w2, bv_t2, at_w2, bank,
-                              m1_w2, m3_w2, zc_w, warm);
-  k_conv12<<<108,512,0,stream>>>(imgTP, W1Tp, W2Tp, WATp, bv_bn1, bv_bn2, iA_bn,
-                                 iepart, i1part);
-  k_mid<<<4,512,0,stream>>>(totApart,a0A,aLA,totBpart,a0B,aLB, rmspart, tA_w2, bv_t2,
-                            i1part, iepart,
-                            at_w1, at_b1, at_ln_g, at_ln_b, at_w2, at_b2, protos,
-                            bv_w1, bv_b1, bv_ln_g, bv_ln_b, bv_w2, bv_b2, bank,
-                            m1_w1, m1_b1, m1_ln_g, m1_ln_b,
-                            m3_w1, m3_b1, m3_ln_g, m3_ln_b,
-                            idxp, hid1, hid3);
+                              m1_w2, m3_w2, zc_w, warm, donec);
+  k_cm<<<112,512,0,stream>>>(imgTP, W1Tp, W2Tp, WATp, bv_bn1, bv_bn2, iA_bn,
+                             iepart, i1part,
+                             totApart, a0A, aLA, totBpart, a0B, aLB, rmspart,
+                             tA_w2, bv_t2,
+                             at_w1, at_b1, at_ln_g, at_ln_b, at_w2, at_b2, protos,
+                             bv_w1, bv_b1, bv_ln_g, bv_ln_b, bv_w2, bv_b2, bank,
+                             m1_w1, m1_b1, m1_ln_g, m1_ln_b,
+                             m3_w1, m3_b1, m3_ln_g, m3_ln_b,
+                             idxp, hid1, hid3, donec);
   k_heads<<<160,256,0,stream>>>(hid1, hid3, m1_w2, m1_b2, m3_w2, m3_b2, A1p, A3p);
   k_dynF<<<192,512,0,stream>>>(imgTP, A1p, A3p, idxp, blr_bn, zc_w, zc_b, img_f, (float*)d_out);
 
```
